# Optimization experiments

Hardware: AMD Instinct MI355X
Metric: run time of the kernel (lower is better)

Reference implementation:

```python
import jax, jax.numpy as jnp
import numpy as np

B, DIM, H, HD, DS = 256, 1024, 16, 64, 4
NL, NKV = HD, HD * DS  # mask shape constraint: num_tok_q == head_dim, num_tok_kv == head_dim*downscaling
EPS = 1e-5


def _ln(t, g, b):
    m = t.mean(-1, keepdims=True)
    v = ((t - m) ** 2).mean(-1, keepdims=True)
    return (t - m) / jnp.sqrt(v + EPS) * g + b


def setup_inputs() -> dict:
    key = jax.random.key(0)
    ks = jax.random.split(key, 7)
    s = DIM ** -0.5
    return {
        'x': jax.random.normal(ks[0], (B, NKV, DIM), jnp.float32),
        'latents': jax.random.normal(ks[1], (B, NL, DIM), jnp.float32),
        'Wq': jax.random.normal(ks[2], (DIM, DIM), jnp.float32) * s,
        'Wk': jax.random.normal(ks[3], (DIM, DIM), jnp.float32) * s,
        'Wv': jax.random.normal(ks[4], (DIM, DIM), jnp.float32) * s,
        'Wo': jax.random.normal(ks[5], (DIM, DIM), jnp.float32) * s,
        'bo': jnp.zeros((DIM,), jnp.float32),
        'g_out': jnp.ones((DIM,), jnp.float32),
        'b_out': jnp.zeros((DIM,), jnp.float32),
        'g_x': jnp.ones((DIM,), jnp.float32),
        'b_x': jnp.zeros((DIM,), jnp.float32),
        'g_l': jnp.ones((DIM,), jnp.float32),
        'b_l': jnp.zeros((DIM,), jnp.float32),
    }


def reference(x, latents, Wq, Wk, Wv, Wo, bo, g_out, b_out, g_x, b_x, g_l, b_l):
    # pre-norms
    ln_l = _ln(latents, g_l, b_l)   # (B, NL, DIM) -> queries
    ln_x = _ln(x, g_x, b_x)         # (B, NKV, DIM) -> keys/values
    # QKV projections (torch Linear: y = x @ W.T), split heads: b n (h d) -> b h n d
    q = (ln_l @ Wq.T).reshape(B, NL, H, HD).transpose(0, 2, 1, 3)
    k = (ln_x @ Wk.T).reshape(B, NKV, H, HD).transpose(0, 2, 1, 3)
    v = (ln_x @ Wv.T).reshape(B, NKV, H, HD).transpose(0, 2, 1, 3)
    qk = jnp.einsum('bhid,bhjd->bhij', q, k) * (HD ** -0.5)  # (B,H,NL,NKV)
    # faithful to original: (HD,HD) strict-upper -inf mask, repeat_interleave by DS along kv axis
    mask = jnp.triu(jnp.full((HD, HD), -jnp.inf, jnp.float32), k=1)
    mask = jnp.repeat(mask, DS, axis=1)  # (NL, NKV)
    attn = jax.nn.softmax(qk + mask[None, None], axis=-1)
    out = jnp.einsum('bhij,bhjd->bhid', attn, v)
    out = out.transpose(0, 2, 1, 3).reshape(B, NL, DIM)  # b h n d -> b n (h d)
    out = _ln(out, g_out, b_out)      # norm_out (hard-coded True)
    out = out @ Wo.T + bo             # to_out; dropout p=0 -> identity
    return latents + out              # residual=True
```

## Files before the change

### kernel.cpp

```cpp
#include <hip/hip_runtime.h>


typedef unsigned short u16;
typedef float f32x4 __attribute__((ext_vector_type(4)));
typedef short bf16x8 __attribute__((ext_vector_type(8)));
typedef u16 u16x4 __attribute__((ext_vector_type(4)));

#define DEV __device__ __forceinline__

DEV u16 f2bf(float f) {
  union { float f; unsigned int u; } c; c.f = f;
  unsigned int u = c.u;
  u += 0x7fffu + ((u >> 16) & 1u);
  return (u16)(u >> 16);
}
DEV float bf2f(u16 u) {
  union { unsigned int u; float f; } c; c.u = ((unsigned int)u) << 16; return c.f;
}
DEV f32x4 mfma16(bf16x8 a, bf16x8 b, f32x4 c) {
  return __builtin_amdgcn_mfma_f32_16x16x32_bf16(a, b, c, 0, 0, 0);
}
DEV void gl16(const void* g, void* l) {
  __builtin_amdgcn_global_load_lds((const __attribute__((address_space(1))) void*)g,
                                   (__attribute__((address_space(3))) void*)l, 16, 0, 0);
}

DEV void ln_row_f32(const float* __restrict__ srcrow, const float* __restrict__ g,
                    const float* __restrict__ bta, u16* __restrict__ dstrow,
                    int tid, float* red) {
  const float4 r = *((const float4*)srcrow + tid);
  float v[4] = {r.x, r.y, r.z, r.w};
  float s = v[0] + v[1] + v[2] + v[3];
  float q = v[0]*v[0] + v[1]*v[1] + v[2]*v[2] + v[3]*v[3];
#pragma unroll
  for (int off = 32; off; off >>= 1) {
    s += __shfl_xor(s, off, 64);
    q += __shfl_xor(q, off, 64);
  }
  if ((tid & 63) == 0) { red[(tid >> 6) * 2] = s; red[(tid >> 6) * 2 + 1] = q; }
  __syncthreads();
  s = red[0] + red[2] + red[4] + red[6];
  q = red[1] + red[3] + red[5] + red[7];
  const float mean = s * (1.f / 1024.f);
  const float rstd = rsqrtf(q * (1.f / 1024.f) - mean * mean + 1e-5f);
  const float4 gv = *((const float4*)g + tid);
  const float4 bv = *((const float4*)bta + tid);
  u16x4 o;
  o[0] = f2bf((v[0] - mean) * rstd * gv.x + bv.x);
  o[1] = f2bf((v[1] - mean) * rstd * gv.y + bv.y);
  o[2] = f2bf((v[2] - mean) * rstd * gv.z + bv.z);
  o[3] = f2bf((v[3] - mean) * rstd * gv.w + bv.w);
  *((u16x4*)dstrow + tid) = o;
}

__global__ __launch_bounds__(256) void fused_pre(const float* __restrict__ w0,
                                                 const float* __restrict__ w1,
                                                 const float* __restrict__ w2,
                                                 const float* __restrict__ w3,
                                                 u16* __restrict__ wout,
                                                 const float* __restrict__ lat,
                                                 const float* __restrict__ g_l,
                                                 const float* __restrict__ b_l,
                                                 u16* __restrict__ lnl,
                                                 const float* __restrict__ x,
                                                 const float* __restrict__ g_x,
                                                 const float* __restrict__ b_x,
                                                 u16* __restrict__ lnx) {
  __shared__ float red[8];
  const int bid = blockIdx.x, tid = threadIdx.x;
  if (bid < 4096) {
    const int g = bid >> 10;
    const float* src = (g == 0) ? w0 : (g == 1) ? w1 : (g == 2) ? w2 : w3;
    const int i = ((bid & 1023) * 256 + tid) * 4;
    const float4 v = *(const float4*)(src + i);
    u16x4 o; o[0] = f2bf(v.x); o[1] = f2bf(v.y); o[2] = f2bf(v.z); o[3] = f2bf(v.w);
    *(u16x4*)(wout + (size_t)g * 1048576 + i) = o;
  } else if (bid < 20480) {
    const int row = bid - 4096;
    ln_row_f32(lat + (size_t)row * 1024, g_l, b_l, lnl + (size_t)row * 1024, tid, red);
  } else {
    const int row = bid - 20480;
    ln_row_f32(x + (size_t)row * 1024, g_x, b_x, lnx + (size_t)row * 1024, tid, red);
  }
}

__global__ __launch_bounds__(256) void ln_bf(const u16* __restrict__ src,
                                             const float* __restrict__ g,
                                             const float* __restrict__ bta,
                                             u16* __restrict__ dst) {
  const int row = blockIdx.x, tid = threadIdx.x;
  const u16x4 r = *((const u16x4*)(src + (size_t)row * 1024) + tid);
  float v[4];
#pragma unroll
  for (int i = 0; i < 4; ++i) v[i] = bf2f(r[i]);
  float s = v[0] + v[1] + v[2] + v[3];
  float q = v[0]*v[0] + v[1]*v[1] + v[2]*v[2] + v[3]*v[3];
#pragma unroll
  for (int off = 32; off; off >>= 1) {
    s += __shfl_xor(s, off, 64);
    q += __shfl_xor(q, off, 64);
  }
  __shared__ float red[8];
  if ((tid & 63) == 0) { red[(tid >> 6) * 2] = s; red[(tid >> 6) * 2 + 1] = q; }
  __syncthreads();
  s = red[0] + red[2] + red[4] + red[6];
  q = red[1] + red[3] + red[5] + red[7];
  const float mean = s * (1.f / 1024.f);
  const float rstd = rsqrtf(q * (1.f / 1024.f) - mean * mean + 1e-5f);
  const float4 gv = *((const float4*)g + tid);
  const float4 bv = *((const float4*)bta + tid);
  u16x4 o;
  o[0] = f2bf((v[0] - mean) * rstd * gv.x + bv.x);
  o[1] = f2bf((v[1] - mean) * rstd * gv.y + bv.y);
  o[2] = f2bf((v[2] - mean) * rstd * gv.z + bv.z);
  o[3] = f2bf((v[3] - mean) * rstd * gv.w + bv.w);
  *((u16x4*)(dst + (size_t)row * 1024) + tid) = o;
}

DEV void gemm_core(const u16* __restrict__ Asrc, const u16* __restrict__ Bsrc,
                   u16 (&As)[2][16384], u16 (&Bs)[2][16384],
                   const int (&goff)[4], const int (&loff)[4], const int (&chk)[2],
                   int wm, int wn, int fr, f32x4 (&acc)[8][4]) {
  constexpr int NT = 16;

#define STG_A(buf, kt, h) { gl16(Asrc + (size_t)(kt) * 64 + goff[2*(h)],     &As[buf][loff[2*(h)]]); \
                            gl16(Asrc + (size_t)(kt) * 64 + goff[2*(h)+1],   &As[buf][loff[2*(h)+1]]); }
#define STG_B(buf, kt, h) { gl16(Bsrc + (size_t)(kt) * 64 + goff[2*(h)],     &Bs[buf][loff[2*(h)]]); \
                            gl16(Bsrc + (size_t)(kt) * 64 + goff[2*(h)+1],   &Bs[buf][loff[2*(h)+1]]); }
#define LDA(H) _Pragma("unroll") for (int mp = 0; mp < 4; ++mp) \
               _Pragma("unroll") for (int ks = 0; ks < 2; ++ks) \
                 af[mp][ks] = *(const bf16x8*)&Ab[(wm * 128 + ((H)*4 + mp) * 16 + fr) * 64 + chk[ks]];
#define LDB(DST, G) _Pragma("unroll") for (int np = 0; np < 2; ++np) \
                    _Pragma("unroll") for (int ks = 0; ks < 2; ++ks) \
                      DST[np][ks] = *(const bf16x8*)&Bb[(wn * 64 + ((G)*2 + np) * 16 + fr) * 64 + chk[ks]];
#define MFMA_Q(H, BF, G) _Pragma("unroll") for (int mp = 0; mp < 4; ++mp) \
                         _Pragma("unroll") for (int np = 0; np < 2; ++np) \
                         _Pragma("unroll") for (int ks = 0; ks < 2; ++ks) \
                           acc[(H)*4 + mp][(G)*2 + np] = mfma16(af[mp][ks], BF[np][ks], acc[(H)*4 + mp][(G)*2 + np]);

  STG_A(0, 0, 0); STG_A(0, 0, 1);
  STG_B(0, 0, 0); STG_B(0, 0, 1);
  STG_A(1, 1, 0); STG_A(1, 1, 1);
  asm volatile("s_waitcnt vmcnt(4)" ::: "memory");
  __builtin_amdgcn_s_barrier();

  for (int t = 0; t < NT; ++t) {
    const int bsel = t & 1;
    const u16* Ab = As[bsel];
    const u16* Bb = Bs[bsel];
    bf16x8 af[4][2], bfrA[2][2], bfrB[2][2];
    LDA(0); LDB(bfrA, 0);
    if (t + 1 < NT) STG_B(bsel ^ 1, t + 1, 0);
    __builtin_amdgcn_s_barrier();
    asm volatile("s_waitcnt lgkmcnt(0)" ::: "memory");
    __builtin_amdgcn_s_setprio(1);
    MFMA_Q(0, bfrA, 0);
    __builtin_amdgcn_s_setprio(0);
    __builtin_amdgcn_s_barrier();
    LDB(bfrB, 1);
    if (t + 1 < NT) STG_B(bsel ^ 1, t + 1, 1);
    __builtin_amdgcn_s_barrier();
    asm volatile("s_waitcnt lgkmcnt(0)" ::: "memory");
    __builtin_amdgcn_s_setprio(1);
    MFMA_Q(0, bfrB, 1);
    __builtin_amdgcn_s_setprio(0);
    __builtin_amdgcn_s_barrier();
    LDA(1);
    __builtin_amdgcn_s_barrier();
    asm volatile("s_waitcnt lgkmcnt(0)" ::: "memory");
    __builtin_amdgcn_s_setprio(1);
    MFMA_Q(1, bfrB, 1);
    __builtin_amdgcn_s_setprio(0);
    __builtin_amdgcn_s_barrier();
    if (t + 2 < NT) { STG_A(bsel, t + 2, 0); STG_A(bsel, t + 2, 1); }
    __builtin_amdgcn_s_setprio(1);
    MFMA_Q(1, bfrA, 0);
    __builtin_amdgcn_s_setprio(0);
    if (t + 2 < NT) asm volatile("s_waitcnt vmcnt(4)" ::: "memory");
    else            asm volatile("s_waitcnt vmcnt(0)" ::: "memory");
    __builtin_amdgcn_s_barrier();
  }
#undef STG_A
#undef STG_B
#undef LDA
#undef LDB
#undef MFMA_Q
}

DEV void gemm_prep(int tid, int lane, int (&goff)[4], int (&loff)[4], int (&chk)[2],
                   f32x4 (&acc)[8][4]) {
#pragma unroll
  for (int i = 0; i < 4; ++i) {
    const int s = i * 512 + tid;
    const int gr = s >> 3, gc = (s & 7) ^ (gr & 7);
    goff[i] = gr * 1024 + gc * 8;
    loff[i] = s * 8;
  }
  const int fq = lane >> 4;
#pragma unroll
  for (int ks = 0; ks < 2; ++ks) chk[ks] = ((((ks << 2) + fq)) ^ (lane & 7)) * 8;
  const f32x4 z = {0.f, 0.f, 0.f, 0.f};
#pragma unroll
  for (int m = 0; m < 8; ++m)
#pragma unroll
    for (int n = 0; n < 4; ++n) acc[m][n] = z;
}

__global__ __launch_bounds__(512, 2) void gemm_qkv(const u16* __restrict__ A0,
                                                   const u16* __restrict__ A1,
                                                   const u16* __restrict__ Bkv,
                                                   const u16* __restrict__ Bq,
                                                   u16* __restrict__ kb,
                                                   u16* __restrict__ vt,
                                                   u16* __restrict__ qb) {
  __shared__ u16 As[2][16384];
  __shared__ u16 Bs[2][16384];
  const int tid = threadIdx.x, lane = tid & 63, wid = tid >> 6;
  const int wm = wid >> 2, wn = wid & 3;
  const int q8 = (int)gridDim.x >> 3;
  const int wg = ((int)blockIdx.x & 7) * q8 + ((int)blockIdx.x >> 3);
  const bool isQ = wg >= 2048;
  const int wg0 = isQ ? wg - 2048 : wg;
  const int tiles_n = isQ ? 4 : 8;
  const int tn = wg0 % tiles_n, tm = wg0 / tiles_n;

  const u16* Asrc = (isQ ? A1 : A0) + (size_t)tm * 262144;
  const u16* Bsrc = (isQ ? Bq : Bkv) + (size_t)tn * 262144;

  int goff[4], loff[4], chk[2];
  f32x4 acc[8][4];
  gemm_prep(tid, lane, goff, loff, chk, acc);
  gemm_core(Asrc, Bsrc, As, Bs, goff, loff, chk, wm, wn, lane & 15, acc);

  const int fr = lane & 15, fq = lane >> 4;
  if (isQ) {
#pragma unroll
    for (int m = 0; m < 8; ++m) {
      const int r0 = tm * 256 + wm * 128 + m * 16 + fq * 4;
      const int b = r0 >> 6, i0 = r0 & 63;
#pragma unroll
      for (int n = 0; n < 4; ++n) {
        const int c = tn * 256 + wn * 64 + n * 16 + fr;
        const int h = c >> 6, d = c & 63;
        u16* p = qb + ((size_t)(b * 16 + h) * 64 + i0) * 64 + d;
#pragma unroll
        for (int j = 0; j < 4; ++j) p[j * 64] = f2bf(acc[m][n][j]);
      }
    }
  } else if (tn < 4) {
#pragma unroll
    for (int m = 0; m < 8; ++m) {
      const int t0 = wm * 128 + m * 16 + fq * 4;
#pragma unroll
      for (int n = 0; n < 4; ++n) {
        const int c = tn * 256 + wn * 64 + n * 16 + fr;
        const int h = c >> 6, d = c & 63;
        u16* p = kb + ((size_t)(tm * 16 + h) * 256 + t0) * 64 + d;
#pragma unroll
        for (int j = 0; j < 4; ++j) p[j * 64] = f2bf(acc[m][n][j]);
      }
    }
  } else {
#pragma unroll
    for (int m = 0; m < 8; ++m) {
      const int t0 = wm * 128 + m * 16 + fq * 4;
#pragma unroll
      for (int n = 0; n < 4; ++n) {
        const int c = (tn - 4) * 256 + wn * 64 + n * 16 + fr;
        const int h = c >> 6, d = c & 63;
        u16x4 o;
#pragma unroll
        for (int j = 0; j < 4; ++j) o[j] = f2bf(acc[m][n][j]);
        *(u16x4*)(vt + ((size_t)(tm * 16 + h) * 64 + d) * 256 + t0) = o;
      }
    }
  }
}

__global__ __launch_bounds__(512, 2) void gemm_out(const u16* __restrict__ A,
                                                   const u16* __restrict__ Bo,
                                                   const float* __restrict__ bias,
                                                   const float* __restrict__ resid,
                                                   float* __restrict__ outf) {
  __shared__ u16 As[2][16384];
  __shared__ u16 Bs[2][16384];
  const int tid = threadIdx.x, lane = tid & 63, wid = tid >> 6;
  const int wm = wid >> 2, wn = wid & 3;
  const int q8 = (int)gridDim.x >> 3;
  const int wg = ((int)blockIdx.x & 7) * q8 + ((int)blockIdx.x >> 3);
  const int tn = wg % 4, tm = wg / 4;

  const u16* Asrc = A + (size_t)tm * 262144;
  const u16* Bsrc = Bo + (size_t)tn * 262144;

  int goff[4], loff[4], chk[2];
  f32x4 acc[8][4];
  gemm_prep(tid, lane, goff, loff, chk, acc);
  gemm_core(Asrc, Bsrc, As, Bs, goff, loff, chk, wm, wn, lane & 15, acc);

  const int fr = lane & 15, fq = lane >> 4;
#pragma unroll
  for (int m = 0; m < 8; ++m) {
    const int r0 = tm * 256 + wm * 128 + m * 16 + fq * 4;
#pragma unroll
    for (int n = 0; n < 4; ++n) {
      const int c = tn * 256 + wn * 64 + n * 16 + fr;
      const float bc = bias[c];
#pragma unroll
      for (int j = 0; j < 4; ++j) {
        const size_t idx = (size_t)(r0 + j) * 1024 + c;
        outf[idx] = acc[m][n][j] + bc + resid[idx];
      }
    }
  }
}

__global__ __launch_bounds__(256) void attn_kernel(const u16* __restrict__ Qb,
                                                   const u16* __restrict__ Kb,
                                                   const u16* __restrict__ Vt,
                                                   u16* __restrict__ AO) {
  __shared__ u16 Qs[64 * 64];
  __shared__ u16 Ks[256 * 64];
  __shared__ u16 Vs[64 * 256];
  const int bh = blockIdx.x;
  const int tid = threadIdx.x, lane = tid & 63, wv = tid >> 6;
  const u16* qsrc = Qb + (size_t)bh * 4096;
  const u16* ksrc = Kb + (size_t)bh * 16384;
  const u16* vsrc = Vt + (size_t)bh * 16384;
#pragma unroll
  for (int i = 0; i < 2; ++i) gl16(qsrc + (i * 256 + tid) * 8, &Qs[(i * 256 + tid) * 8]);
#pragma unroll
  for (int i = 0; i < 8; ++i) gl16(ksrc + (i * 256 + tid) * 8, &Ks[(i * 256 + tid) * 8]);
#pragma unroll
  for (int i = 0; i < 8; ++i) gl16(vsrc + (i * 256 + tid) * 8, &Vs[(i * 256 + tid) * 8]);
  asm volatile("s_waitcnt vmcnt(8)" ::: "memory");
  __builtin_amdgcn_s_barrier();

  f32x4 sacc[16];
  const f32x4 z = {0.f, 0.f, 0.f, 0.f};
#pragma unroll
  for (int n = 0; n < 16; ++n) sacc[n] = z;
#pragma unroll
  for (int s = 0; s < 2; ++s) {
    const bf16x8 aq = *(const bf16x8*)&Qs[(wv * 16 + (lane & 15)) * 64 + s * 32 + (lane >> 4) * 8];
#pragma unroll
    for (int n = 0; n < 16; ++n) {
      const bf16x8 bk = *(const bf16x8*)&Ks[(n * 16 + (lane & 15)) * 64 + s * 32 + (lane >> 4) * 8];
      sacc[n] = mfma16(aq, bk, sacc[n]);
    }
  }

  const int rgrp = lane >> 4, cl = lane & 15;
  float inv[4];
#pragma unroll
  for (int j = 0; j < 4; ++j) {
    const int qrow = (wv << 4) + (rgrp << 2) + j;
    float m_ = -1e30f;
#pragma unroll
    for (int n = 0; n < 16; ++n) {
      const int col = (n << 4) + cl;
      float sv = sacc[n][j] * 0.125f;
      sv = ((col >> 2) <= qrow) ? sv : -1e30f;
      sacc[n][j] = sv;
      m_ = fmaxf(m_, sv);
    }
#pragma unroll
    for (int off = 8; off; off >>= 1) m_ = fmaxf(m_, __shfl_xor(m_, off, 64));
    float s_ = 0.f;
#pragma unroll
    for (int n = 0; n < 16; ++n) {
      const float p = exp2f((sacc[n][j] - m_) * 1.44269504f);
      sacc[n][j] = p;
      s_ += p;
    }
#pragma unroll
    for (int off = 8; off; off >>= 1) s_ += __shfl_xor(s_, off, 64);
    inv[j] = 1.0f / s_;
  }

  asm volatile("s_waitcnt vmcnt(0)" ::: "memory");
  __builtin_amdgcn_s_barrier();
  u16* Ps = Ks;
#pragma unroll
  for (int n = 0; n < 16; ++n)
#pragma unroll
    for (int j = 0; j < 4; ++j)
      Ps[((wv << 4) + (rgrp << 2) + j) * 256 + (n << 4) + cl] = f2bf(sacc[n][j]);
  __syncthreads();

  f32x4 oacc[4];
#pragma unroll
  for (int n = 0; n < 4; ++n) oacc[n] = z;
#pragma unroll
  for (int ks = 0; ks < 8; ++ks) {
    const bf16x8 ap = *(const bf16x8*)&Ps[(wv * 16 + (lane & 15)) * 256 + ks * 32 + (lane >> 4) * 8];
#pragma unroll
    for (int n = 0; n < 4; ++n) {
      const bf16x8 bv = *(const bf16x8*)&Vs[(n * 16 + (lane & 15)) * 256 + ks * 32 + (lane >> 4) * 8];
      oacc[n] = mfma16(ap, bv, oacc[n]);
    }
  }
  const int b = bh >> 4, h = bh & 15;
  u16* obase = AO + (size_t)b * 65536 + (size_t)h * 64;
#pragma unroll
  for (int n = 0; n < 4; ++n)
#pragma unroll
    for (int j = 0; j < 4; ++j) {
      const int qrow = (wv << 4) + (rgrp << 2) + j;
      const int d = (n << 4) + cl;
      obase[(size_t)qrow * 1024 + d] = f2bf(oacc[n][j] * inv[j]);
    }
}

extern "C" void kernel_launch(void* const* d_in, const int* in_sizes, int n_in,
                              void* d_out, int out_size, void* d_ws, size_t ws_size,
                              hipStream_t stream) {
  const float* x     = (const float*)d_in[0];
  const float* lat   = (const float*)d_in[1];
  const float* Wq    = (const float*)d_in[2];
  const float* Wk    = (const float*)d_in[3];
  const float* Wv    = (const float*)d_in[4];
  const float* Wo    = (const float*)d_in[5];
  const float* bo    = (const float*)d_in[6];
  const float* g_out = (const float*)d_in[7];
  const float* b_out = (const float*)d_in[8];
  const float* g_x   = (const float*)d_in[9];
  const float* b_x   = (const float*)d_in[10];
  const float* g_l   = (const float*)d_in[11];
  const float* b_l   = (const float*)d_in[12];
  float* out = (float*)d_out;

  char* W = (char*)d_ws;
  u16* wqb = (u16*)(W + 0);
  u16* wkb = (u16*)(W + 2097152);
  u16* wvb = (u16*)(W + 4194304);
  u16* wob = (u16*)(W + 6291456);
  u16* lnl = (u16*)(W + 8388608);
  u16* lnx = (u16*)(W + 41943040);
  u16* qb  = (u16*)(W + 176160768);
  u16* kb  = (u16*)(W + 209715200);
  u16* vt  = (u16*)(W + 343932928);
  u16* ao  = lnx;
  u16* lna = qb;
  (void)wvb;

  fused_pre<<<86016, 256, 0, stream>>>(Wq, Wk, Wv, Wo, wqb,
                                       lat, g_l, b_l, lnl,
                                       x, g_x, b_x, lnx);

  gemm_qkv<<<2304, 512, 0, stream>>>(lnx, lnl, wkb, wqb, kb, vt, qb);

  attn_kernel<<<4096, 256, 0, stream>>>(qb, kb, vt, ao);

  ln_bf<<<16384, 256, 0, stream>>>(ao, g_out, b_out, lna);

  gemm_out<<<256, 512, 0, stream>>>(lna, wob, bo, lat, out);
}
```

Baseline: 623.7 us.

## Fold output LayerNorm into Wo GEMM epilogue and switch GEMMs to 32x32 MFMA

The output LayerNorm is now folded into the final GEMM. g_out is pre-multiplied into the bf16 copy of Wo. A stats kernel computes per-row mean and rstd plus the per-column Wo·g_out and Wo·b_out sums, and the GEMM epilogue applies rs*acc - rs*mean*u + w. This removes the normalized bf16 write and reread of the attention output, at some numerical risk because raw unnormalized values are now fed to the bf16 GEMM. Separately, both GEMMs move from 16x16x32 to 32x32x16 bf16 MFMA with the fragment loads and epilogue indexing reworked, which changes register use and store patterns.

```diff
diff --git a/kernel.cpp b/kernel.cpp
--- a/kernel.cpp
+++ b/kernel.cpp
@@ -3,6 +3,7 @@
 
 typedef unsigned short u16;
 typedef float f32x4 __attribute__((ext_vector_type(4)));
+typedef float f32x16 __attribute__((ext_vector_type(16)));
 typedef short bf16x8 __attribute__((ext_vector_type(8)));
 typedef u16 u16x4 __attribute__((ext_vector_type(4)));
 
@@ -19,6 +20,9 @@
 }
 DEV f32x4 mfma16(bf16x8 a, bf16x8 b, f32x4 c) {
   return __builtin_amdgcn_mfma_f32_16x16x32_bf16(a, b, c, 0, 0, 0);
+}
+DEV f32x16 mfma32(bf16x8 a, bf16x8 b, f32x16 c) {
+  return __builtin_amdgcn_mfma_f32_32x32x16_bf16(a, b, c, 0, 0, 0);
 }
 DEV void gl16(const void* g, void* l) {
   __builtin_amdgcn_global_load_lds((const __attribute__((address_space(1))) void*)g,
@@ -58,6 +62,8 @@
                                                  const float* __restrict__ w2,
                                                  const float* __restrict__ w3,
                                                  u16* __restrict__ wout,
+                                                 u16* __restrict__ wob,
+                                                 const float* __restrict__ g_out,
                                                  const float* __restrict__ lat,
                                                  const float* __restrict__ g_l,
                                                  const float* __restrict__ b_l,
@@ -70,11 +76,20 @@
   const int bid = blockIdx.x, tid = threadIdx.x;
   if (bid < 4096) {
     const int g = bid >> 10;
-    const float* src = (g == 0) ? w0 : (g == 1) ? w1 : (g == 2) ? w2 : w3;
     const int i = ((bid & 1023) * 256 + tid) * 4;
-    const float4 v = *(const float4*)(src + i);
-    u16x4 o; o[0] = f2bf(v.x); o[1] = f2bf(v.y); o[2] = f2bf(v.z); o[3] = f2bf(v.w);
-    *(u16x4*)(wout + (size_t)g * 1048576 + i) = o;
+    if (g < 3) {
+      const float* src = (g == 0) ? w0 : (g == 1) ? w1 : w2;
+      const float4 v = *(const float4*)(src + i);
+      u16x4 o; o[0] = f2bf(v.x); o[1] = f2bf(v.y); o[2] = f2bf(v.z); o[3] = f2bf(v.w);
+      *(u16x4*)(wout + (size_t)g * 1048576 + i) = o;
+    } else {
+      const float4 v = *(const float4*)(w3 + i);
+      const float4 gv = *((const float4*)g_out + tid);
+      u16x4 o;
+      o[0] = f2bf(gv.x * v.x); o[1] = f2bf(gv.y * v.y);
+      o[2] = f2bf(gv.z * v.z); o[3] = f2bf(gv.w * v.w);
+      *(u16x4*)(wob + i) = o;
+    }
   } else if (bid < 20480) {
     const int row = bid - 4096;
     ln_row_f32(lat + (size_t)row * 1024, g_l, b_l, lnl + (size_t)row * 1024, tid, red);
@@ -84,59 +99,74 @@
   }
 }
 
-__global__ __launch_bounds__(256) void ln_bf(const u16* __restrict__ src,
-                                             const float* __restrict__ g,
-                                             const float* __restrict__ bta,
-                                             u16* __restrict__ dst) {
-  const int row = blockIdx.x, tid = threadIdx.x;
-  const u16x4 r = *((const u16x4*)(src + (size_t)row * 1024) + tid);
-  float v[4];
-#pragma unroll
-  for (int i = 0; i < 4; ++i) v[i] = bf2f(r[i]);
-  float s = v[0] + v[1] + v[2] + v[3];
-  float q = v[0]*v[0] + v[1]*v[1] + v[2]*v[2] + v[3]*v[3];
-#pragma unroll
-  for (int off = 32; off; off >>= 1) {
-    s += __shfl_xor(s, off, 64);
-    q += __shfl_xor(q, off, 64);
-  }
+__global__ __launch_bounds__(256) void stats_kernel(const u16* __restrict__ ao,
+                                                    float* __restrict__ meanb,
+                                                    float* __restrict__ rstdb,
+                                                    const float* __restrict__ Wo,
+                                                    const float* __restrict__ g_out,
+                                                    const float* __restrict__ b_out,
+                                                    float* __restrict__ ub,
+                                                    float* __restrict__ wb) {
   __shared__ float red[8];
-  if ((tid & 63) == 0) { red[(tid >> 6) * 2] = s; red[(tid >> 6) * 2 + 1] = q; }
-  __syncthreads();
-  s = red[0] + red[2] + red[4] + red[6];
-  q = red[1] + red[3] + red[5] + red[7];
-  const float mean = s * (1.f / 1024.f);
-  const float rstd = rsqrtf(q * (1.f / 1024.f) - mean * mean + 1e-5f);
-  const float4 gv = *((const float4*)g + tid);
-  const float4 bv = *((const float4*)bta + tid);
-  u16x4 o;
-  o[0] = f2bf((v[0] - mean) * rstd * gv.x + bv.x);
-  o[1] = f2bf((v[1] - mean) * rstd * gv.y + bv.y);
-  o[2] = f2bf((v[2] - mean) * rstd * gv.z + bv.z);
-  o[3] = f2bf((v[3] - mean) * rstd * gv.w + bv.w);
-  *((u16x4*)(dst + (size_t)row * 1024) + tid) = o;
-}
-
-DEV void gemm_core(const u16* __restrict__ Asrc, const u16* __restrict__ Bsrc,
-                   u16 (&As)[2][16384], u16 (&Bs)[2][16384],
-                   const int (&goff)[4], const int (&loff)[4], const int (&chk)[2],
-                   int wm, int wn, int fr, f32x4 (&acc)[8][4]) {
+  const int bid = blockIdx.x, tid = threadIdx.x;
+  if (bid < 16384) {
+    const u16x4 r = *((const u16x4*)(ao + (size_t)bid * 1024) + tid);
+    float v0 = bf2f(r[0]), v1 = bf2f(r[1]), v2 = bf2f(r[2]), v3 = bf2f(r[3]);
+    float s = v0 + v1 + v2 + v3;
+    float q = v0*v0 + v1*v1 + v2*v2 + v3*v3;
+#pragma unroll
+    for (int off = 32; off; off >>= 1) {
+      s += __shfl_xor(s, off, 64);
+      q += __shfl_xor(q, off, 64);
+    }
+    if ((tid & 63) == 0) { red[(tid >> 6) * 2] = s; red[(tid >> 6) * 2 + 1] = q; }
+    __syncthreads();
+    if (tid == 0) {
+      s = red[0] + red[2] + red[4] + red[6];
+      q = red[1] + red[3] + red[5] + red[7];
+      const float m = s * (1.f / 1024.f);
+      meanb[bid] = m;
+      rstdb[bid] = rsqrtf(q * (1.f / 1024.f) - m * m + 1e-5f);
+    }
+  } else {
+    const int c = bid - 16384;
+    const float4 v = *((const float4*)(Wo + (size_t)c * 1024) + tid);
+    const float4 gv = *((const float4*)g_out + tid);
+    const float4 bv = *((const float4*)b_out + tid);
+    float su = gv.x*v.x + gv.y*v.y + gv.z*v.z + gv.w*v.w;
+    float sw = bv.x*v.x + bv.y*v.y + bv.z*v.z + bv.w*v.w;
+#pragma unroll
+    for (int off = 32; off; off >>= 1) {
+      su += __shfl_xor(su, off, 64);
+      sw += __shfl_xor(sw, off, 64);
+    }
+    if ((tid & 63) == 0) { red[(tid >> 6) * 2] = su; red[(tid >> 6) * 2 + 1] = sw; }
+    __syncthreads();
+    if (tid == 0) {
+      ub[c] = red[0] + red[2] + red[4] + red[6];
+      wb[c] = red[1] + red[3] + red[5] + red[7];
+    }
+  }
+}
+
+DEV void gemm_core32(const u16* __restrict__ Asrc, const u16* __restrict__ Bsrc,
+                     u16 (&As)[2][16384], u16 (&Bs)[2][16384],
+                     const int (&goff)[4], const int (&loff)[4], const int (&chk)[4],
+                     int wm, int wn, int cl32, f32x16 (&acc)[4][2]) {
   constexpr int NT = 16;
 
 #define STG_A(buf, kt, h) { gl16(Asrc + (size_t)(kt) * 64 + goff[2*(h)],     &As[buf][loff[2*(h)]]); \
                             gl16(Asrc + (size_t)(kt) * 64 + goff[2*(h)+1],   &As[buf][loff[2*(h)+1]]); }
 #define STG_B(buf, kt, h) { gl16(Bsrc + (size_t)(kt) * 64 + goff[2*(h)],     &Bs[buf][loff[2*(h)]]); \
                             gl16(Bsrc + (size_t)(kt) * 64 + goff[2*(h)+1],   &Bs[buf][loff[2*(h)+1]]); }
-#define LDA(H) _Pragma("unroll") for (int mp = 0; mp < 4; ++mp) \
-               _Pragma("unroll") for (int ks = 0; ks < 2; ++ks) \
-                 af[mp][ks] = *(const bf16x8*)&Ab[(wm * 128 + ((H)*4 + mp) * 16 + fr) * 64 + chk[ks]];
-#define LDB(DST, G) _Pragma("unroll") for (int np = 0; np < 2; ++np) \
-                    _Pragma("unroll") for (int ks = 0; ks < 2; ++ks) \
-                      DST[np][ks] = *(const bf16x8*)&Bb[(wn * 64 + ((G)*2 + np) * 16 + fr) * 64 + chk[ks]];
-#define MFMA_Q(H, BF, G) _Pragma("unroll") for (int mp = 0; mp < 4; ++mp) \
-                         _Pragma("unroll") for (int np = 0; np < 2; ++np) \
-                         _Pragma("unroll") for (int ks = 0; ks < 2; ++ks) \
-                           acc[(H)*4 + mp][(G)*2 + np] = mfma16(af[mp][ks], BF[np][ks], acc[(H)*4 + mp][(G)*2 + np]);
+#define LDA(H) _Pragma("unroll") for (int mp = 0; mp < 2; ++mp) \
+               _Pragma("unroll") for (int ks = 0; ks < 4; ++ks) \
+                 af[mp][ks] = *(const bf16x8*)&Ab[(wm * 128 + ((H)*2 + mp) * 32 + cl32) * 64 + chk[ks]];
+#define LDB(DST, G) _Pragma("unroll") for (int ks = 0; ks < 4; ++ks) \
+                      DST[ks] = *(const bf16x8*)&Bb[(wn * 64 + (G) * 32 + cl32) * 64 + chk[ks]];
+#define MFMA_Q(H, BF, G) _Pragma("unroll") for (int ks = 0; ks < 4; ++ks) \
+                         _Pragma("unroll") for (int mp = 0; mp < 2; ++mp) \
+                           acc[(H)*2 + mp][G] = mfma32(af[mp][ks], BF[ks], acc[(H)*2 + mp][G]);
 
   STG_A(0, 0, 0); STG_A(0, 0, 1);
   STG_B(0, 0, 0); STG_B(0, 0, 1);
@@ -148,7 +178,7 @@
     const int bsel = t & 1;
     const u16* Ab = As[bsel];
     const u16* Bb = Bs[bsel];
-    bf16x8 af[4][2], bfrA[2][2], bfrB[2][2];
+    bf16x8 af[2][4], bfrA[4], bfrB[4];
     LDA(0); LDB(bfrA, 0);
     if (t + 1 < NT) STG_B(bsel ^ 1, t + 1, 0);
     __builtin_amdgcn_s_barrier();
@@ -187,8 +217,8 @@
 #undef MFMA_Q
 }
 
-DEV void gemm_prep(int tid, int lane, int (&goff)[4], int (&loff)[4], int (&chk)[2],
-                   f32x4 (&acc)[8][4]) {
+DEV void gemm_prep32(int tid, int lane, int (&goff)[4], int (&loff)[4], int (&chk)[4],
+                     f32x16 (&acc)[4][2]) {
 #pragma unroll
   for (int i = 0; i < 4; ++i) {
     const int s = i * 512 + tid;
@@ -196,14 +226,15 @@
     goff[i] = gr * 1024 + gc * 8;
     loff[i] = s * 8;
   }
-  const int fq = lane >> 4;
-#pragma unroll
-  for (int ks = 0; ks < 2; ++ks) chk[ks] = ((((ks << 2) + fq)) ^ (lane & 7)) * 8;
-  const f32x4 z = {0.f, 0.f, 0.f, 0.f};
-#pragma unroll
-  for (int m = 0; m < 8; ++m)
-#pragma unroll
-    for (int n = 0; n < 4; ++n) acc[m][n] = z;
+  const int s5 = lane >> 5;
+#pragma unroll
+  for (int ks = 0; ks < 4; ++ks) chk[ks] = (((ks << 1) + s5) ^ (lane & 7)) * 8;
+#pragma unroll
+  for (int m = 0; m < 4; ++m)
+#pragma unroll
+    for (int n = 0; n < 2; ++n)
+#pragma unroll
+      for (int e = 0; e < 16; ++e) acc[m][n][e] = 0.f;
 }
 
 __global__ __launch_bounds__(512, 2) void gemm_qkv(const u16* __restrict__ A0,
@@ -227,51 +258,65 @@
   const u16* Asrc = (isQ ? A1 : A0) + (size_t)tm * 262144;
   const u16* Bsrc = (isQ ? Bq : Bkv) + (size_t)tn * 262144;
 
-  int goff[4], loff[4], chk[2];
-  f32x4 acc[8][4];
-  gemm_prep(tid, lane, goff, loff, chk, acc);
-  gemm_core(Asrc, Bsrc, As, Bs, goff, loff, chk, wm, wn, lane & 15, acc);
-
-  const int fr = lane & 15, fq = lane >> 4;
+  const int cl32 = lane & 31, s5 = lane >> 5;
+  int goff[4], loff[4], chk[4];
+  f32x16 acc[4][2];
+  gemm_prep32(tid, lane, goff, loff, chk, acc);
+  gemm_core32(Asrc, Bsrc, As, Bs, goff, loff, chk, wm, wn, cl32, acc);
+
   if (isQ) {
 #pragma unroll
-    for (int m = 0; m < 8; ++m) {
-      const int r0 = tm * 256 + wm * 128 + m * 16 + fq * 4;
-      const int b = r0 >> 6, i0 = r0 & 63;
-#pragma unroll
-      for (int n = 0; n < 4; ++n) {
-        const int c = tn * 256 + wn * 64 + n * 16 + fr;
+    for (int mb = 0; mb < 4; ++mb) {
+      const int rb = tm * 256 + wm * 128 + mb * 32 + s5 * 4;
+#pragma unroll
+      for (int nb = 0; nb < 2; ++nb) {
+        const int c = tn * 256 + wn * 64 + nb * 32 + cl32;
         const int h = c >> 6, d = c & 63;
-        u16* p = qb + ((size_t)(b * 16 + h) * 64 + i0) * 64 + d;
-#pragma unroll
-        for (int j = 0; j < 4; ++j) p[j * 64] = f2bf(acc[m][n][j]);
+        const f32x16 a = acc[mb][nb];
+#pragma unroll
+        for (int q = 0; q < 4; ++q)
+#pragma unroll
+          for (int j = 0; j < 4; ++j) {
+            const int r = rb + q * 8 + j;
+            const int b = r >> 6, i0 = r & 63;
+            qb[((size_t)(b * 16 + h) * 64 + i0) * 64 + d] = f2bf(a[q * 4 + j]);
+          }
       }
     }
   } else if (tn < 4) {
 #pragma unroll
-    for (int m = 0; m < 8; ++m) {
-      const int t0 = wm * 128 + m * 16 + fq * 4;
-#pragma unroll
-      for (int n = 0; n < 4; ++n) {
-        const int c = tn * 256 + wn * 64 + n * 16 + fr;
+    for (int mb = 0; mb < 4; ++mb) {
+      const int tb = wm * 128 + mb * 32 + s5 * 4;
+#pragma unroll
+      for (int nb = 0; nb < 2; ++nb) {
+        const int c = tn * 256 + wn * 64 + nb * 32 + cl32;
         const int h = c >> 6, d = c & 63;
-        u16* p = kb + ((size_t)(tm * 16 + h) * 256 + t0) * 64 + d;
-#pragma unroll
-        for (int j = 0; j < 4; ++j) p[j * 64] = f2bf(acc[m][n][j]);
+        const f32x16 a = acc[mb][nb];
+#pragma unroll
+        for (int q = 0; q < 4; ++q)
+#pragma unroll
+          for (int j = 0; j < 4; ++j) {
+            const int t = tb + q * 8 + j;
+            kb[((size_t)(tm * 16 + h) * 256 + t) * 64 + d] = f2bf(a[q * 4 + j]);
+          }
       }
     }
   } else {
 #pragma unroll
-    for (int m = 0; m < 8; ++m) {
-      const int t0 = wm * 128 + m * 16 + fq * 4;
-#pragma unroll
-      for (int n = 0; n < 4; ++n) {
-        const int c = (tn - 4) * 256 + wn * 64 + n * 16 + fr;
+    for (int mb = 0; mb < 4; ++mb) {
+      const int tb = wm * 128 + mb * 32 + s5 * 4;
+#pragma unroll
+      for (int nb = 0; nb < 2; ++nb) {
+        const int c = (tn - 4) * 256 + wn * 64 + nb * 32 + cl32;
         const int h = c >> 6, d = c & 63;
-        u16x4 o;
-#pragma unroll
-        for (int j = 0; j < 4; ++j) o[j] = f2bf(acc[m][n][j]);
-        *(u16x4*)(vt + ((size_t)(tm * 16 + h) * 64 + d) * 256 + t0) = o;
+        const f32x16 a = acc[mb][nb];
+#pragma unroll
+        for (int q = 0; q < 4; ++q) {
+          u16x4 o;
+#pragma unroll
+          for (int j = 0; j < 4; ++j) o[j] = f2bf(a[q * 4 + j]);
+          *(u16x4*)(vt + ((size_t)(tm * 16 + h) * 64 + d) * 256 + tb + q * 8) = o;
+        }
       }
     }
   }
@@ -279,7 +324,11 @@
 
 __global__ __launch_bounds__(512, 2) void gemm_out(const u16* __restrict__ A,
                                                    const u16* __restrict__ Bo,
+                                                   const float* __restrict__ ub,
+                                                   const float* __restrict__ wb,
                                                    const float* __restrict__ bias,
+                                                   const float* __restrict__ meanb,
+                                                   const float* __restrict__ rstdb,
                                                    const float* __restrict__ resid,
                                                    float* __restrict__ outf) {
   __shared__ u16 As[2][16384];
@@ -293,24 +342,30 @@
   const u16* Asrc = A + (size_t)tm * 262144;
   const u16* Bsrc = Bo + (size_t)tn * 262144;
 
-  int goff[4], loff[4], chk[2];
-  f32x4 acc[8][4];
-  gemm_prep(tid, lane, goff, loff, chk, acc);
-  gemm_core(Asrc, Bsrc, As, Bs, goff, loff, chk, wm, wn, lane & 15, acc);
-
-  const int fr = lane & 15, fq = lane >> 4;
-#pragma unroll
-  for (int m = 0; m < 8; ++m) {
-    const int r0 = tm * 256 + wm * 128 + m * 16 + fq * 4;
-#pragma unroll
-    for (int n = 0; n < 4; ++n) {
-      const int c = tn * 256 + wn * 64 + n * 16 + fr;
-      const float bc = bias[c];
-#pragma unroll
-      for (int j = 0; j < 4; ++j) {
-        const size_t idx = (size_t)(r0 + j) * 1024 + c;
-        outf[idx] = acc[m][n][j] + bc + resid[idx];
-      }
+  const int cl32 = lane & 31, s5 = lane >> 5;
+  int goff[4], loff[4], chk[4];
+  f32x16 acc[4][2];
+  gemm_prep32(tid, lane, goff, loff, chk, acc);
+  gemm_core32(Asrc, Bsrc, As, Bs, goff, loff, chk, wm, wn, cl32, acc);
+
+#pragma unroll
+  for (int mb = 0; mb < 4; ++mb) {
+    const int rb = tm * 256 + wm * 128 + mb * 32 + s5 * 4;
+#pragma unroll
+    for (int nb = 0; nb < 2; ++nb) {
+      const int c = tn * 256 + wn * 64 + nb * 32 + cl32;
+      const float uc = ub[c];
+      const float wc = wb[c] + bias[c];
+      const f32x16 a = acc[mb][nb];
+#pragma unroll
+      for (int q = 0; q < 4; ++q)
+#pragma unroll
+        for (int j = 0; j < 4; ++j) {
+          const int r = rb + q * 8 + j;
+          const float rs = rstdb[r], mn = meanb[r];
+          const size_t idx = (size_t)r * 1024 + c;
+          outf[idx] = rs * a[q * 4 + j] - rs * mn * uc + wc + resid[idx];
+        }
     }
   }
 }
@@ -441,10 +496,13 @@
   u16* kb  = (u16*)(W + 209715200);
   u16* vt  = (u16*)(W + 343932928);
   u16* ao  = lnx;
-  u16* lna = qb;
+  float* meanb = (float*)qb;
+  float* rstdb = (float*)((char*)qb + 65536);
+  float* ub    = (float*)((char*)qb + 131072);
+  float* wb    = (float*)((char*)qb + 135168);
   (void)wvb;
 
-  fused_pre<<<86016, 256, 0, stream>>>(Wq, Wk, Wv, Wo, wqb,
+  fused_pre<<<86016, 256, 0, stream>>>(Wq, Wk, Wv, Wo, wqb, wob, g_out,
                                        lat, g_l, b_l, lnl,
                                        x, g_x, b_x, lnx);
 
@@ -452,7 +510,7 @@
 
   attn_kernel<<<4096, 256, 0, stream>>>(qb, kb, vt, ao);
 
-  ln_bf<<<16384, 256, 0, stream>>>(ao, g_out, b_out, lna);
-
-  gemm_out<<<256, 512, 0, stream>>>(lna, wob, bo, lat, out);
-}
+  stats_kernel<<<17408, 256, 0, stream>>>(ao, meanb, rstdb, Wo, g_out, b_out, ub, wb);
+
+  gemm_out<<<256, 512, 0, stream>>>(ao, wob, ub, wb, bo, meanb, rstdb, lat, out);
+}
```

Measured after the change: 648.1 us. 3.9% more time.

## Fold output LayerNorm into the output GEMM epilogue using row statistics

Applied to the files above, without the earlier changes.

Replaces the separate output LayerNorm pass, which wrote a normalized bf16 activation buffer, with a stats kernel. That kernel computes only the per-row mean and rstd, plus per-column sums of gamma*Wo and beta*Wo. The gamma scaling is folded into the bf16 Wo conversion. The output GEMM now consumes the raw attention output and applies the normalization algebraically in its epilogue. This removes a full-size activation write and its re-read, at the cost of a less accurate result: centering happens after bf16 matmul accumulation, and the column sums come from fp32 weights while the GEMM uses bf16 weights.

```diff
diff --git a/kernel.cpp b/kernel.cpp
--- a/kernel.cpp
+++ b/kernel.cpp
@@ -58,6 +58,8 @@
                                                  const float* __restrict__ w2,
                                                  const float* __restrict__ w3,
                                                  u16* __restrict__ wout,
+                                                 u16* __restrict__ wob,
+                                                 const float* __restrict__ g_out,
                                                  const float* __restrict__ lat,
                                                  const float* __restrict__ g_l,
                                                  const float* __restrict__ b_l,
@@ -70,11 +72,20 @@
   const int bid = blockIdx.x, tid = threadIdx.x;
   if (bid < 4096) {
     const int g = bid >> 10;
-    const float* src = (g == 0) ? w0 : (g == 1) ? w1 : (g == 2) ? w2 : w3;
     const int i = ((bid & 1023) * 256 + tid) * 4;
-    const float4 v = *(const float4*)(src + i);
-    u16x4 o; o[0] = f2bf(v.x); o[1] = f2bf(v.y); o[2] = f2bf(v.z); o[3] = f2bf(v.w);
-    *(u16x4*)(wout + (size_t)g * 1048576 + i) = o;
+    if (g < 3) {
+      const float* src = (g == 0) ? w0 : (g == 1) ? w1 : w2;
+      const float4 v = *(const float4*)(src + i);
+      u16x4 o; o[0] = f2bf(v.x); o[1] = f2bf(v.y); o[2] = f2bf(v.z); o[3] = f2bf(v.w);
+      *(u16x4*)(wout + (size_t)g * 1048576 + i) = o;
+    } else {
+      const float4 v = *(const float4*)(w3 + i);
+      const float4 gv = *((const float4*)g_out + tid);
+      u16x4 o;
+      o[0] = f2bf(gv.x * v.x); o[1] = f2bf(gv.y * v.y);
+      o[2] = f2bf(gv.z * v.z); o[3] = f2bf(gv.w * v.w);
+      *(u16x4*)(wob + i) = o;
+    }
   } else if (bid < 20480) {
     const int row = bid - 4096;
     ln_row_f32(lat + (size_t)row * 1024, g_l, b_l, lnl + (size_t)row * 1024, tid, red);
@@ -84,37 +95,54 @@
   }
 }
 
-__global__ __launch_bounds__(256) void ln_bf(const u16* __restrict__ src,
-                                             const float* __restrict__ g,
-                                             const float* __restrict__ bta,
-                                             u16* __restrict__ dst) {
-  const int row = blockIdx.x, tid = threadIdx.x;
-  const u16x4 r = *((const u16x4*)(src + (size_t)row * 1024) + tid);
-  float v[4];
-#pragma unroll
-  for (int i = 0; i < 4; ++i) v[i] = bf2f(r[i]);
-  float s = v[0] + v[1] + v[2] + v[3];
-  float q = v[0]*v[0] + v[1]*v[1] + v[2]*v[2] + v[3]*v[3];
-#pragma unroll
-  for (int off = 32; off; off >>= 1) {
-    s += __shfl_xor(s, off, 64);
-    q += __shfl_xor(q, off, 64);
-  }
+__global__ __launch_bounds__(256) void stats_kernel(const u16* __restrict__ ao,
+                                                    float* __restrict__ meanb,
+                                                    float* __restrict__ rstdb,
+                                                    const float* __restrict__ Wo,
+                                                    const float* __restrict__ g_out,
+                                                    const float* __restrict__ b_out,
+                                                    float* __restrict__ ub,
+                                                    float* __restrict__ wb) {
   __shared__ float red[8];
-  if ((tid & 63) == 0) { red[(tid >> 6) * 2] = s; red[(tid >> 6) * 2 + 1] = q; }
-  __syncthreads();
-  s = red[0] + red[2] + red[4] + red[6];
-  q = red[1] + red[3] + red[5] + red[7];
-  const float mean = s * (1.f / 1024.f);
-  const float rstd = rsqrtf(q * (1.f / 1024.f) - mean * mean + 1e-5f);
-  const float4 gv = *((const float4*)g + tid);
-  const float4 bv = *((const float4*)bta + tid);
-  u16x4 o;
-  o[0] = f2bf((v[0] - mean) * rstd * gv.x + bv.x);
-  o[1] = f2bf((v[1] - mean) * rstd * gv.y + bv.y);
-  o[2] = f2bf((v[2] - mean) * rstd * gv.z + bv.z);
-  o[3] = f2bf((v[3] - mean) * rstd * gv.w + bv.w);
-  *((u16x4*)(dst + (size_t)row * 1024) + tid) = o;
+  const int bid = blockIdx.x, tid = threadIdx.x;
+  if (bid < 16384) {
+    const u16x4 r = *((const u16x4*)(ao + (size_t)bid * 1024) + tid);
+    float v0 = bf2f(r[0]), v1 = bf2f(r[1]), v2 = bf2f(r[2]), v3 = bf2f(r[3]);
+    float s = v0 + v1 + v2 + v3;
+    float q = v0*v0 + v1*v1 + v2*v2 + v3*v3;
+#pragma unroll
+    for (int off = 32; off; off >>= 1) {
+      s += __shfl_xor(s, off, 64);
+      q += __shfl_xor(q, off, 64);
+    }
+    if ((tid & 63) == 0) { red[(tid >> 6) * 2] = s; red[(tid >> 6) * 2 + 1] = q; }
+    __syncthreads();
+    if (tid == 0) {
+      s = red[0] + red[2] + red[4] + red[6];
+      q = red[1] + red[3] + red[5] + red[7];
+      const float m = s * (1.f / 1024.f);
+      meanb[bid] = m;
+      rstdb[bid] = rsqrtf(q * (1.f / 1024.f) - m * m + 1e-5f);
+    }
+  } else {
+    const int c = bid - 16384;
+    const float4 v = *((const float4*)(Wo + (size_t)c * 1024) + tid);
+    const float4 gv = *((const float4*)g_out + tid);
+    const float4 bv = *((const float4*)b_out + tid);
+    float su = gv.x*v.x + gv.y*v.y + gv.z*v.z + gv.w*v.w;
+    float sw = bv.x*v.x + bv.y*v.y + bv.z*v.z + bv.w*v.w;
+#pragma unroll
+    for (int off = 32; off; off >>= 1) {
+      su += __shfl_xor(su, off, 64);
+      sw += __shfl_xor(sw, off, 64);
+    }
+    if ((tid & 63) == 0) { red[(tid >> 6) * 2] = su; red[(tid >> 6) * 2 + 1] = sw; }
+    __syncthreads();
+    if (tid == 0) {
+      ub[c] = red[0] + red[2] + red[4] + red[6];
+      wb[c] = red[1] + red[3] + red[5] + red[7];
+    }
+  }
 }
 
 DEV void gemm_core(const u16* __restrict__ Asrc, const u16* __restrict__ Bsrc,
@@ -279,7 +307,11 @@
 
 __global__ __launch_bounds__(512, 2) void gemm_out(const u16* __restrict__ A,
                                                    const u16* __restrict__ Bo,
+                                                   const float* __restrict__ ub,
+                                                   const float* __restrict__ wb,
                                                    const float* __restrict__ bias,
+                                                   const float* __restrict__ meanb,
+                                                   const float* __restrict__ rstdb,
                                                    const float* __restrict__ resid,
                                                    float* __restrict__ outf) {
   __shared__ u16 As[2][16384];
@@ -305,11 +337,14 @@
 #pragma unroll
     for (int n = 0; n < 4; ++n) {
       const int c = tn * 256 + wn * 64 + n * 16 + fr;
-      const float bc = bias[c];
+      const float uc = ub[c];
+      const float wc = wb[c] + bias[c];
 #pragma unroll
       for (int j = 0; j < 4; ++j) {
-        const size_t idx = (size_t)(r0 + j) * 1024 + c;
-        outf[idx] = acc[m][n][j] + bc + resid[idx];
+        const int r = r0 + j;
+        const float rs = rstdb[r], mn = meanb[r];
+        const size_t idx = (size_t)r * 1024 + c;
+        outf[idx] = rs * acc[m][n][j] - rs * mn * uc + wc + resid[idx];
       }
     }
   }
@@ -441,10 +476,13 @@
   u16* kb  = (u16*)(W + 209715200);
   u16* vt  = (u16*)(W + 343932928);
   u16* ao  = lnx;
-  u16* lna = qb;
+  float* meanb = (float*)qb;
+  float* rstdb = (float*)((char*)qb + 65536);
+  float* ub    = (float*)((char*)qb + 131072);
+  float* wb    = (float*)((char*)qb + 135168);
   (void)wvb;
 
-  fused_pre<<<86016, 256, 0, stream>>>(Wq, Wk, Wv, Wo, wqb,
+  fused_pre<<<86016, 256, 0, stream>>>(Wq, Wk, Wv, Wo, wqb, wob, g_out,
                                        lat, g_l, b_l, lnl,
                                        x, g_x, b_x, lnx);
 
@@ -452,7 +490,7 @@
 
   attn_kernel<<<4096, 256, 0, stream>>>(qb, kb, vt, ao);
 
-  ln_bf<<<16384, 256, 0, stream>>>(ao, g_out, b_out, lna);
-
-  gemm_out<<<256, 512, 0, stream>>>(lna, wob, bo, lat, out);
-}
+  stats_kernel<<<17408, 256, 0, stream>>>(ao, meanb, rstdb, Wo, g_out, b_out, ub, wb);
+
+  gemm_out<<<256, 512, 0, stream>>>(ao, wob, ub, wb, bo, meanb, rstdb, lat, out);
+}
```

Measured after the change: 620.0 us. About the same (-0.6%).
